# Performance work log

Measured on AMD Instinct MI355X. Metric: run time of the kernel, lower is better.

## Reference

```python
import jax, jax.numpy as jnp
import numpy as np

N = 200000          # total nodes across the batch of graphs
IN_DIM = 320        # pooling_dim (256) + num_context_attrs (64)
POOL_DIM = 256      # output_dim
HID = 128
NUM_GRAPHS = 2000


def setup_inputs() -> dict:
    key = jax.random.key(0)
    k = jax.random.split(key, 6)
    z = jax.random.normal(k[0], (N, IN_DIM), dtype=jnp.float32)
    batch_index = jnp.sort(jax.random.randint(k[1], (N,), 0, NUM_GRAPHS, dtype=jnp.int64))
    # Kaiming-ish small init to keep softmax well-conditioned
    W1 = jax.random.normal(k[2], (HID, IN_DIM), dtype=jnp.float32) * (1.0 / np.sqrt(IN_DIM))
    b1 = jax.random.normal(k[3], (HID,), dtype=jnp.float32) * 0.01
    W2 = jax.random.normal(k[4], (1, HID), dtype=jnp.float32) * (1.0 / np.sqrt(HID))
    b2 = jax.random.normal(k[5], (1,), dtype=jnp.float32) * 0.01
    return {"z": z, "batch_index": batch_index, "W1": W1, "b1": b1,
            "W2": W2, "b2": b2, "num_graphs": NUM_GRAPHS}


def reference(z, batch_index, W1, b1, W2, b2, num_graphs):
    # attention_net: Linear -> ReLU -> Linear, scores: [N, 1]
    h = jax.nn.relu(z @ W1.T + b1)                  # [N, HID]
    scores = h @ W2.T + b2                          # [N, 1]
    # global (over all nodes) max-subtract + softmax along dim 0
    scores = scores - jnp.max(scores, axis=0, keepdims=True)
    weights = jax.nn.softmax(scores, axis=0)        # [N, 1]
    # weighted scatter-mean over graphs keyed by batch_index
    weighted = weights * z[:, :POOL_DIM]            # [N, POOL_DIM]
    sums = jax.ops.segment_sum(weighted, batch_index, num_segments=num_graphs)  # [G, POOL_DIM]
    counts = jax.ops.segment_sum(jnp.ones((z.shape[0],), dtype=z.dtype),
                                 batch_index, num_segments=num_graphs)          # [G]
    pooled = sums / jnp.maximum(counts, 1.0)[:, None]
    return pooled
```

## Files before the change

kernel.cpp:

```cpp
#include <hip/hip_runtime.h>

#define IN_DIM   320
#define POOL_DIM 256
#define HID      128
#define RPB      128
#define NKC      10

typedef __attribute__((ext_vector_type(8))) short bf16x8;
typedef __attribute__((ext_vector_type(4))) float f32x4;

typedef __attribute__((address_space(1))) const unsigned int guint;
typedef __attribute__((address_space(3))) unsigned int luint;

__device__ __forceinline__ void gl_lds16(const void* g, void* l) {
    __builtin_amdgcn_global_load_lds((guint*)g, (luint*)l, 16, 0, 0);
}

__device__ __forceinline__ unsigned fbits(float f) {
    union { float f; unsigned u; } c; c.f = f; return c.u;
}
__device__ __forceinline__ unsigned pack2(unsigned u0, unsigned u1) {
    return __builtin_amdgcn_perm(u1, u0, 0x07060302u);
}

__device__ __forceinline__ void split8(float4 a, float4 b, bf16x8& hi, bf16x8& lo) {
    float f[8] = { a.x, a.y, a.z, a.w, b.x, b.y, b.z, b.w };
    unsigned hu[8], lu[8];
#pragma unroll
    for (int i = 0; i < 8; ++i) {
        unsigned u = fbits(f[i]);
        hu[i] = u;
        float hif = __builtin_bit_cast(float, u & 0xffff0000u);
        lu[i] = fbits(f[i] - hif);
    }
    int4 hp, lp;
    hp.x = pack2(hu[0], hu[1]); hp.y = pack2(hu[2], hu[3]);
    hp.z = pack2(hu[4], hu[5]); hp.w = pack2(hu[6], hu[7]);
    lp.x = pack2(lu[0], lu[1]); lp.y = pack2(lu[2], lu[3]);
    lp.z = pack2(lu[4], lu[5]); lp.w = pack2(lu[6], lu[7]);
    hi = __builtin_bit_cast(bf16x8, hp);
    lo = __builtin_bit_cast(bf16x8, lp);
}

__global__ __launch_bounds__(256) void pack_w1_kernel(
    const float* __restrict__ W1, ushort* __restrict__ Wpk)
{
    const int i = blockIdx.x * 256 + threadIdx.x;
    if (i >= NKC * 8 * 2 * 64) return;
    const int kc   = i >> 10;
    const int r    = i & 1023;
    const int ht   = r >> 7;
    const int r2   = r & 127;
    const int s    = r2 >> 6;
    const int lane = r2 & 63;
    const int h    = ht * 16 + (lane & 15);
    const int k0   = kc * 32 + (lane >> 4) * 8;

    ushort v[8];
#pragma unroll
    for (int j = 0; j < 8; ++j) {
        const float f = W1[(size_t)h * IN_DIM + k0 + j];
        const unsigned u = fbits(f);
        if (s == 0) {
            v[j] = (ushort)(u >> 16);
        } else {
            const float hif = __builtin_bit_cast(float, u & 0xffff0000u);
            v[j] = (ushort)(fbits(f - hif) >> 16);
        }
    }
    ushort* dst = Wpk + (size_t)i * 8;
#pragma unroll
    for (int j = 0; j < 8; ++j) dst[j] = v[j];
}

__global__ __launch_bounds__(256) void attn_scores_mfma(
    const float* __restrict__ z, const ushort* __restrict__ Wpk,
    const float* __restrict__ b1, const float* __restrict__ W2,
    const float* __restrict__ b2,
    float* __restrict__ scores, float* __restrict__ bmax,
    float* __restrict__ bsum, int N)
{
    __shared__ float4 wbuf[2][1024];
    __shared__ float  sblk[RPB];

    const int tid  = threadIdx.x;
    const int wid  = tid >> 6;
    const int lane = tid & 63;
    const int lm   = lane & 15;
    const int lg   = lane >> 4;
    const int r0   = blockIdx.x * RPB;
    const int wr0  = r0 + wid * 32;

    int row0 = wr0 + lm;      if (row0 > N - 1) row0 = N - 1;
    int row1 = wr0 + 16 + lm; if (row1 > N - 1) row1 = N - 1;
    const float* zp0 = z + (size_t)row0 * IN_DIM + lg * 8;
    const float* zp1 = z + (size_t)row1 * IN_DIM + lg * 8;

    #define STAGE_W(kc_, b_)                                                  \
        { const char* src = (const char*)Wpk + (size_t)(kc_) * 16384;         \
          char* dst = (char*)&wbuf[b_][0];                                    \
          _Pragma("unroll")                                                   \
          for (int j = 0; j < 4; ++j) {                                       \
              const int o = (tid + j * 256) * 16;                             \
              gl_lds16(src + o, dst + o);                                     \
          } }

    f32x4 acc[2][8];
#pragma unroll
    for (int rt = 0; rt < 2; ++rt)
#pragma unroll
        for (int ht = 0; ht < 8; ++ht) acc[rt][ht] = (f32x4){0.f, 0.f, 0.f, 0.f};

    float4 zraw[2][4];
    bf16x8 af[2][4];

    STAGE_W(0, 0);

    {
        const float4* p0 = (const float4*)zp0;
        const float4* p1 = (const float4*)zp1;
        zraw[0][0] = p0[0]; zraw[0][1] = p0[1];
        zraw[0][2] = p1[0]; zraw[0][3] = p1[1];
        const float4* q0 = (const float4*)(zp0 + 32);
        const float4* q1 = (const float4*)(zp1 + 32);
        zraw[1][0] = q0[0]; zraw[1][1] = q0[1];
        zraw[1][2] = q1[0]; zraw[1][3] = q1[1];
        split8(zraw[0][0], zraw[0][1], af[0][0], af[0][1]);
        split8(zraw[0][2], zraw[0][3], af[0][2], af[0][3]);
    }
    __syncthreads();

#pragma unroll
    for (int kc = 0; kc < NKC; ++kc) {
        const int cb  = kc & 1;
        const int nb2 = cb ^ 1;

        if (kc + 1 < NKC) STAGE_W(kc + 1, nb2);

        const char* wb_base = (const char*)&wbuf[cb][0] + lane * 16;
#pragma unroll
        for (int ht = 0; ht < 8; ++ht) {
            const bf16x8 bh = *(const bf16x8*)(wb_base + ht * 2048);
            const bf16x8 bl = *(const bf16x8*)(wb_base + ht * 2048 + 1024);
            acc[0][ht] = __builtin_amdgcn_mfma_f32_16x16x32_bf16(af[cb][0], bh, acc[0][ht], 0, 0, 0);
            acc[0][ht] = __builtin_amdgcn_mfma_f32_16x16x32_bf16(af[cb][1], bh, acc[0][ht], 0, 0, 0);
            acc[0][ht] = __builtin_amdgcn_mfma_f32_16x16x32_bf16(af[cb][0], bl, acc[0][ht], 0, 0, 0);
            acc[1][ht] = __builtin_amdgcn_mfma_f32_16x16x32_bf16(af[cb][2], bh, acc[1][ht], 0, 0, 0);
            acc[1][ht] = __builtin_amdgcn_mfma_f32_16x16x32_bf16(af[cb][3], bh, acc[1][ht], 0, 0, 0);
            acc[1][ht] = __builtin_amdgcn_mfma_f32_16x16x32_bf16(af[cb][2], bl, acc[1][ht], 0, 0, 0);
        }

        if (kc + 2 < NKC) {
            const int ko2 = (kc + 2) * 32;
            const float4* p0 = (const float4*)(zp0 + ko2);
            const float4* p1 = (const float4*)(zp1 + ko2);
            zraw[cb][0] = p0[0]; zraw[cb][1] = p0[1];
            zraw[cb][2] = p1[0]; zraw[cb][3] = p1[1];
        }

        if (kc + 1 < NKC) {
            split8(zraw[nb2][0], zraw[nb2][1], af[nb2][0], af[nb2][1]);
            split8(zraw[nb2][2], zraw[nb2][3], af[nb2][2], af[nb2][3]);
            __syncthreads();
        }
    }

    float b1v[8], w2v[8];
#pragma unroll
    for (int ht = 0; ht < 8; ++ht) {
        b1v[ht] = b1[ht * 16 + lm];
        w2v[ht] = W2[ht * 16 + lm];
    }
    const float b2v = b2[0];

#pragma unroll
    for (int rt = 0; rt < 2; ++rt) {
#pragma unroll
        for (int reg = 0; reg < 4; ++reg) {
            float s = 0.f;
#pragma unroll
            for (int ht = 0; ht < 8; ++ht)
                s += fmaxf(acc[rt][ht][reg] + b1v[ht], 0.f) * w2v[ht];
            s += __shfl_xor(s, 1);
            s += __shfl_xor(s, 2);
            s += __shfl_xor(s, 4);
            s += __shfl_xor(s, 8);
            s += b2v;
            if (lm == 0) {
                const int rloc = wid * 32 + rt * 16 + lg * 4 + reg;
                const int grow = r0 + rloc;
                if (grow < N) {
                    scores[grow] = s;
                    sblk[rloc] = s;
                } else {
                    sblk[rloc] = -1e30f;
                }
            }
        }
    }
    __syncthreads();

    if (tid < 64) {
        const float v0 = sblk[tid];
        const float v1 = sblk[tid + 64];
        float m = fmaxf(v0, v1);
#pragma unroll
        for (int d = 1; d < 64; d <<= 1) m = fmaxf(m, __shfl_xor(m, d, 64));
        float e = __expf(v0 - m) + __expf(v1 - m);
#pragma unroll
        for (int d = 1; d < 64; d <<= 1) e += __shfl_xor(e, d, 64);
        if (tid == 0) {
            bmax[blockIdx.x] = m;
            bsum[blockIdx.x] = e;
        }
    }
}

__global__ __launch_bounds__(256) void softmax_reduce_kernel(
    const float* __restrict__ bmax, const float* __restrict__ bsum,
    float* __restrict__ red, int nb)
{
    __shared__ float sm[4];
    __shared__ float ss[4];
    const int tid = threadIdx.x;

    float m = -1e30f;
    for (int i = tid; i < nb; i += 256) m = fmaxf(m, bmax[i]);
#pragma unroll
    for (int d = 1; d < 64; d <<= 1) m = fmaxf(m, __shfl_xor(m, d, 64));
    if ((tid & 63) == 0) sm[tid >> 6] = m;
    __syncthreads();
    const float gmax = fmaxf(fmaxf(sm[0], sm[1]), fmaxf(sm[2], sm[3]));

    float s = 0.f;
    for (int i = tid; i < nb; i += 256) s += bsum[i] * __expf(bmax[i] - gmax);
#pragma unroll
    for (int d = 1; d < 64; d <<= 1) s += __shfl_xor(s, d, 64);
    if ((tid & 63) == 0) ss[tid >> 6] = s;
    __syncthreads();
    if (tid == 0) {
        red[0] = gmax;
        red[1] = ss[0] + ss[1] + ss[2] + ss[3];
    }
}

__device__ __forceinline__ int lower_bound(const int* __restrict__ a, int n, int key)
{
    int lo = 0, hi = n;
    while (lo < hi) {
        int mid = (lo + hi) >> 1;
        if (a[mid] < key) lo = mid + 1; else hi = mid;
    }
    return lo;
}

__global__ __launch_bounds__(256) void pool_kernel(
    const float* __restrict__ z, const int* __restrict__ bidx,
    const float* __restrict__ scores, const float* __restrict__ red,
    float* __restrict__ out, int N)
{
    const int g    = blockIdx.x;
    const int lane = threadIdx.x & 63;
    const int rg   = threadIdx.x >> 6;
    __shared__ int se[2];
    __shared__ f32x4 pred[4][64];

    if (threadIdx.x == 0) {
        se[0] = lower_bound(bidx, N, g);
        se[1] = lower_bound(bidx, N, g + 1);
    }
    __syncthreads();
    const int start = se[0], end = se[1];
    const float gmax    = red[0];
    const float inv_den = 1.0f / red[1];

    const f32x4* zf = (const f32x4*)z;

    f32x4 acc = (f32x4){0.f, 0.f, 0.f, 0.f};
    for (int i = start + rg; i < end; i += 4) {
        const float w = __expf(scores[i] - gmax);
        acc += w * zf[(size_t)i * 80 + lane];
    }
    pred[rg][lane] = acc;
    __syncthreads();

    if (rg == 0) {
        const f32x4 s = (pred[0][lane] + pred[1][lane]) +
                        (pred[2][lane] + pred[3][lane]);
        const int cnt = end - start;
        const float sc = inv_den / fmaxf((float)cnt, 1.0f);
        ((f32x4*)out)[(size_t)g * 64 + lane] = s * sc;
    }
}

extern "C" void kernel_launch(void* const* d_in, const int* in_sizes, int n_in,
                              void* d_out, int out_size, void* d_ws, size_t ws_size,
                              hipStream_t stream)
{
    const float* z    = (const float*)d_in[0];
    const int*   bidx = (const int*)  d_in[1];
    const float* W1   = (const float*)d_in[2];
    const float* b1   = (const float*)d_in[3];
    const float* W2   = (const float*)d_in[4];
    const float* b2   = (const float*)d_in[5];
    float*       out  = (float*)d_out;

    const int N  = in_sizes[0] / IN_DIM;
    const int G  = out_size / POOL_DIM;
    const int nb = (N + RPB - 1) / RPB;

    float*  scores = (float*)d_ws;
    float*  bmax   = scores + 200000;
    float*  bsum   = bmax + 1600;
    float*  red    = bsum + 1600;
    ushort* Wpk    = (ushort*)(red + 16);

    pack_w1_kernel<<<(NKC * 8 * 2 * 64 + 255) / 256, 256, 0, stream>>>(W1, Wpk);
    attn_scores_mfma<<<nb, 256, 0, stream>>>(z, Wpk, b1, W2, b2,
                                             scores, bmax, bsum, N);
    softmax_reduce_kernel<<<1, 256, 0, stream>>>(bmax, bsum, red, nb);
    pool_kernel<<<G, 256, 0, stream>>>(z, bidx, scores, red, out, N);
}
```

Baseline: 110.4 us.

## Fuse weighted segment pooling into score kernel with per-block partials

The score kernel now uses the block's sorted batch indices to find graph segments and accumulates exp-weighted partial sums of the pooled features while z rows are still hot. It writes the per-segment partials plus graph ids. A small combine kernel rescales each partial by its block max relative to the global max and sums them per graph. This avoids a second full pass over z in the pool kernel, at the cost of partial-buffer traffic and a serial segment loop per block.

```diff
diff --git a/kernel.cpp b/kernel.cpp
--- a/kernel.cpp
+++ b/kernel.cpp
@@ -5,6 +5,7 @@
 #define HID      128
 #define RPB      128
 #define NKC      10
+#define NSEG     16
 
 typedef __attribute__((ext_vector_type(8))) short bf16x8;
 typedef __attribute__((ext_vector_type(4))) float f32x4;
@@ -73,15 +74,20 @@
     for (int j = 0; j < 8; ++j) dst[j] = v[j];
 }
 
-__global__ __launch_bounds__(256) void attn_scores_mfma(
+__global__ __launch_bounds__(256) void attn_fused(
     const float* __restrict__ z, const ushort* __restrict__ Wpk,
     const float* __restrict__ b1, const float* __restrict__ W2,
-    const float* __restrict__ b2,
-    float* __restrict__ scores, float* __restrict__ bmax,
-    float* __restrict__ bsum, int N)
+    const float* __restrict__ b2, const int* __restrict__ bidx,
+    float* __restrict__ bmax, float* __restrict__ bsum,
+    float* __restrict__ P, int* __restrict__ meta, int N)
 {
     __shared__ float4 wbuf[2][1024];
     __shared__ float  sblk[RPB];
+    __shared__ int    gbid[RPB];
+    __shared__ int    seg_s0[RPB + 1];
+    __shared__ int    seg_gid[RPB];
+    __shared__ int    scnt[2];
+    __shared__ float  mshare;
 
     const int tid  = threadIdx.x;
     const int wid  = tid >> 6;
@@ -90,6 +96,7 @@
     const int lg   = lane >> 4;
     const int r0   = blockIdx.x * RPB;
     const int wr0  = r0 + wid * 32;
+    const int nvalid = (N - r0 < RPB) ? (N - r0) : RPB;
 
     int row0 = wr0 + lm;      if (row0 > N - 1) row0 = N - 1;
     int row1 = wr0 + 16 + lm; if (row1 > N - 1) row1 = N - 1;
@@ -188,13 +195,7 @@
             s += b2v;
             if (lm == 0) {
                 const int rloc = wid * 32 + rt * 16 + lg * 4 + reg;
-                const int grow = r0 + rloc;
-                if (grow < N) {
-                    scores[grow] = s;
-                    sblk[rloc] = s;
-                } else {
-                    sblk[rloc] = -1e30f;
-                }
+                sblk[rloc] = (rloc < nvalid) ? s : -1e30f;
             }
         }
     }
@@ -212,8 +213,53 @@
         if (tid == 0) {
             bmax[blockIdx.x] = m;
             bsum[blockIdx.x] = e;
-        }
-    }
+            mshare = m;
+        }
+    }
+    if (tid >= 128 && tid < 256) {
+        const int row = tid - 128;
+        gbid[row] = (row < nvalid) ? bidx[r0 + row] : -2;
+    }
+    __syncthreads();
+
+    int flag = 0, idx = 0;
+    if (tid < 128) {
+        const int prev = (tid == 0) ? -999999 : gbid[tid - 1];
+        flag = (gbid[tid] != prev) ? 1 : 0;
+        const unsigned long long mask = __ballot(flag);
+        idx = __popcll(mask & ((1ull << (tid & 63)) - 1ull));
+        if ((tid & 63) == 0) scnt[tid >> 6] = (int)__popcll(mask);
+    }
+    __syncthreads();
+    const int nseg = scnt[0] + scnt[1];
+    if (tid < 128 && flag) {
+        const int pos = idx + ((tid >= 64) ? scnt[0] : 0);
+        seg_s0[pos]  = tid;
+        seg_gid[pos] = gbid[tid];
+    }
+    if (tid == 0) seg_s0[nseg] = RPB;
+    __syncthreads();
+
+    const int rg    = tid >> 6;
+    const float mb  = mshare;
+    const f32x4* zf = (const f32x4*)z;
+    f32x4* P4 = (f32x4*)P;
+
+    for (int s = 0; s < nseg && s < NSEG; ++s) {
+        const int gid = seg_gid[s];
+        if (gid < 0) continue;
+        const int rs = seg_s0[s];
+        const int re = seg_s0[s + 1];
+        f32x4 a = (f32x4){0.f, 0.f, 0.f, 0.f};
+        for (int row = rs + rg; row < re; row += 4) {
+            const float w = __expf(sblk[row] - mb);
+            a += w * zf[(size_t)(r0 + row) * 80 + lane];
+        }
+        P4[(((size_t)blockIdx.x * NSEG + s) * 4 + rg) * 64 + lane] = a;
+    }
+    if (tid < NSEG)
+        meta[blockIdx.x * NSEG + tid] =
+            (tid < nseg && tid < NSEG) ? seg_gid[tid] : -1;
 }
 
 __global__ __launch_bounds__(256) void softmax_reduce_kernel(
@@ -254,43 +300,39 @@
     return lo;
 }
 
-__global__ __launch_bounds__(256) void pool_kernel(
-    const float* __restrict__ z, const int* __restrict__ bidx,
-    const float* __restrict__ scores, const float* __restrict__ red,
-    float* __restrict__ out, int N)
+__global__ __launch_bounds__(64) void combine_kernel(
+    const int* __restrict__ bidx, const float* __restrict__ bmax,
+    const float* __restrict__ red, const float* __restrict__ P,
+    const int* __restrict__ meta, float* __restrict__ out, int N)
 {
     const int g    = blockIdx.x;
-    const int lane = threadIdx.x & 63;
-    const int rg   = threadIdx.x >> 6;
-    __shared__ int se[2];
-    __shared__ f32x4 pred[4][64];
-
-    if (threadIdx.x == 0) {
-        se[0] = lower_bound(bidx, N, g);
-        se[1] = lower_bound(bidx, N, g + 1);
-    }
-    __syncthreads();
-    const int start = se[0], end = se[1];
+    const int lane = threadIdx.x;
+
+    const int start = lower_bound(bidx, N, g);
+    const int end   = lower_bound(bidx, N, g + 1);
     const float gmax    = red[0];
     const float inv_den = 1.0f / red[1];
 
-    const f32x4* zf = (const f32x4*)z;
-
-    f32x4 acc = (f32x4){0.f, 0.f, 0.f, 0.f};
-    for (int i = start + rg; i < end; i += 4) {
-        const float w = __expf(scores[i] - gmax);
-        acc += w * zf[(size_t)i * 80 + lane];
-    }
-    pred[rg][lane] = acc;
-    __syncthreads();
-
-    if (rg == 0) {
-        const f32x4 s = (pred[0][lane] + pred[1][lane]) +
-                        (pred[2][lane] + pred[3][lane]);
-        const int cnt = end - start;
-        const float sc = inv_den / fmaxf((float)cnt, 1.0f);
-        ((f32x4*)out)[(size_t)g * 64 + lane] = s * sc;
-    }
+    f32x4 a = (f32x4){0.f, 0.f, 0.f, 0.f};
+    if (end > start) {
+        const int b0 = start >> 7;
+        const int b1 = (end - 1) >> 7;
+        const f32x4* P4 = (const f32x4*)P;
+        for (int b = b0; b <= b1; ++b) {
+            int s = -1;
+#pragma unroll
+            for (int k = 0; k < NSEG; ++k)
+                if (meta[b * NSEG + k] == g) s = k;
+            if (s < 0) continue;
+            const size_t base = (((size_t)b * NSEG + s) * 4) * 64 + lane;
+            const f32x4 t = (P4[base] + P4[base + 64]) +
+                            (P4[base + 128] + P4[base + 192]);
+            a += __expf(bmax[b] - gmax) * t;
+        }
+    }
+    const int cnt = end - start;
+    const float sc = inv_den / fmaxf((float)cnt, 1.0f);
+    ((f32x4*)out)[(size_t)g * 64 + lane] = a * sc;
 }
 
 extern "C" void kernel_launch(void* const* d_in, const int* in_sizes, int n_in,
@@ -309,15 +351,16 @@
     const int G  = out_size / POOL_DIM;
     const int nb = (N + RPB - 1) / RPB;
 
-    float*  scores = (float*)d_ws;
-    float*  bmax   = scores + 200000;
-    float*  bsum   = bmax + 1600;
-    float*  red    = bsum + 1600;
-    ushort* Wpk    = (ushort*)(red + 16);
+    float*  bmax = (float*)d_ws;
+    float*  bsum = bmax + 1600;
+    float*  red  = bsum + 1600;
+    int*    meta = (int*)(red + 16);
+    float*  P    = (float*)(meta + 1600 * NSEG);
+    ushort* Wpk  = (ushort*)(P + (size_t)1600 * NSEG * 4 * 256);
 
     pack_w1_kernel<<<(NKC * 8 * 2 * 64 + 255) / 256, 256, 0, stream>>>(W1, Wpk);
-    attn_scores_mfma<<<nb, 256, 0, stream>>>(z, Wpk, b1, W2, b2,
-                                             scores, bmax, bsum, N);
+    attn_fused<<<nb, 256, 0, stream>>>(z, Wpk, b1, W2, b2, bidx,
+                                       bmax, bsum, P, meta, N);
     softmax_reduce_kernel<<<1, 256, 0, stream>>>(bmax, bsum, red, nb);
-    pool_kernel<<<G, 256, 0, stream>>>(z, bidx, scores, red, out, N);
-}
+    combine_kernel<<<G, 64, 0, stream>>>(bidx, bmax, red, P, meta, out, N);
+}
```

Result: slower. 122.5 us (+11.0%).

## Stage z tiles into LDS via async global_load_lds with XOR swizzle

Applied to the files above, without the earlier changes.

Moves the z activation loads from per-lane register prefetch into double-buffered LDS staging with direct global-to-LDS loads, using coalesced row-contiguous copies and an XOR swizzle to avoid bank conflicts on readback. Each k-chunk then reads its fragments from LDS and splits them to bf16 hi/lo before the MFMAs. This is meant to improve global coalescing and cut register pressure from the raw prefetch buffers. In exchange it adds 32KB of LDS per block, which may lower occupancy, and puts the split on the critical path after each barrier.

```diff
diff --git a/kernel.cpp b/kernel.cpp
--- a/kernel.cpp
+++ b/kernel.cpp
@@ -81,6 +81,7 @@
     float* __restrict__ bsum, int N)
 {
     __shared__ float4 wbuf[2][1024];
+    __shared__ float4 zbuf[2][1024];
     __shared__ float  sblk[RPB];
 
     const int tid  = threadIdx.x;
@@ -89,12 +90,16 @@
     const int lm   = lane & 15;
     const int lg   = lane >> 4;
     const int r0   = blockIdx.x * RPB;
-    const int wr0  = r0 + wid * 32;
-
-    int row0 = wr0 + lm;      if (row0 > N - 1) row0 = N - 1;
-    int row1 = wr0 + 16 + lm; if (row1 > N - 1) row1 = N - 1;
-    const float* zp0 = z + (size_t)row0 * IN_DIM + lg * 8;
-    const float* zp1 = z + (size_t)row1 * IN_DIM + lg * 8;
+
+    const char* zsrc[4];
+#pragma unroll
+    for (int j = 0; j < 4; ++j) {
+        const int s   = tid + j * 256;
+        const int row = s >> 3;
+        const int q   = (s & 7) ^ (row & 7);
+        int gr = r0 + row; if (gr > N - 1) gr = N - 1;
+        zsrc[j] = (const char*)z + (size_t)gr * (IN_DIM * 4) + q * 16;
+    }
 
     #define STAGE_W(kc_, b_)                                                  \
         { const char* src = (const char*)Wpk + (size_t)(kc_) * 16384;         \
@@ -105,29 +110,29 @@
               gl_lds16(src + o, dst + o);                                     \
           } }
 
+    #define STAGE_Z(kc_, b_)                                                  \
+        { char* dst = (char*)&zbuf[b_][0];                                    \
+          _Pragma("unroll")                                                   \
+          for (int j = 0; j < 4; ++j) {                                       \
+              const int o = (tid + j * 256) * 16;                             \
+              gl_lds16(zsrc[j] + (kc_) * 128, dst + o);                       \
+          } }
+
     f32x4 acc[2][8];
 #pragma unroll
     for (int rt = 0; rt < 2; ++rt)
 #pragma unroll
         for (int ht = 0; ht < 8; ++ht) acc[rt][ht] = (f32x4){0.f, 0.f, 0.f, 0.f};
 
-    float4 zraw[2][4];
-    bf16x8 af[2][4];
-
+    const int lr0 = wid * 32 + lm;
+    const int lr1 = lr0 + 16;
+    const int i00 = lr0 * 8 + ((2 * lg)     ^ (lr0 & 7));
+    const int i01 = lr0 * 8 + ((2 * lg + 1) ^ (lr0 & 7));
+    const int i10 = lr1 * 8 + ((2 * lg)     ^ (lr1 & 7));
+    const int i11 = lr1 * 8 + ((2 * lg + 1) ^ (lr1 & 7));
+
+    STAGE_Z(0, 0);
     STAGE_W(0, 0);
-
-    {
-        const float4* p0 = (const float4*)zp0;
-        const float4* p1 = (const float4*)zp1;
-        zraw[0][0] = p0[0]; zraw[0][1] = p0[1];
-        zraw[0][2] = p1[0]; zraw[0][3] = p1[1];
-        const float4* q0 = (const float4*)(zp0 + 32);
-        const float4* q1 = (const float4*)(zp1 + 32);
-        zraw[1][0] = q0[0]; zraw[1][1] = q0[1];
-        zraw[1][2] = q1[0]; zraw[1][3] = q1[1];
-        split8(zraw[0][0], zraw[0][1], af[0][0], af[0][1]);
-        split8(zraw[0][2], zraw[0][3], af[0][2], af[0][3]);
-    }
     __syncthreads();
 
 #pragma unroll
@@ -135,34 +140,36 @@
         const int cb  = kc & 1;
         const int nb2 = cb ^ 1;
 
-        if (kc + 1 < NKC) STAGE_W(kc + 1, nb2);
+        if (kc + 1 < NKC) {
+            STAGE_Z(kc + 1, nb2);
+            STAGE_W(kc + 1, nb2);
+        }
+
+        bf16x8 a0h, a0l, a1h, a1l;
+        {
+            const float4* zb = &zbuf[cb][0];
+            const float4 x0 = zb[i00];
+            const float4 x1 = zb[i01];
+            const float4 y0 = zb[i10];
+            const float4 y1 = zb[i11];
+            split8(x0, x1, a0h, a0l);
+            split8(y0, y1, a1h, a1l);
+        }
 
         const char* wb_base = (const char*)&wbuf[cb][0] + lane * 16;
 #pragma unroll
         for (int ht = 0; ht < 8; ++ht) {
             const bf16x8 bh = *(const bf16x8*)(wb_base + ht * 2048);
             const bf16x8 bl = *(const bf16x8*)(wb_base + ht * 2048 + 1024);
-            acc[0][ht] = __builtin_amdgcn_mfma_f32_16x16x32_bf16(af[cb][0], bh, acc[0][ht], 0, 0, 0);
-            acc[0][ht] = __builtin_amdgcn_mfma_f32_16x16x32_bf16(af[cb][1], bh, acc[0][ht], 0, 0, 0);
-            acc[0][ht] = __builtin_amdgcn_mfma_f32_16x16x32_bf16(af[cb][0], bl, acc[0][ht], 0, 0, 0);
-            acc[1][ht] = __builtin_amdgcn_mfma_f32_16x16x32_bf16(af[cb][2], bh, acc[1][ht], 0, 0, 0);
-            acc[1][ht] = __builtin_amdgcn_mfma_f32_16x16x32_bf16(af[cb][3], bh, acc[1][ht], 0, 0, 0);
-            acc[1][ht] = __builtin_amdgcn_mfma_f32_16x16x32_bf16(af[cb][2], bl, acc[1][ht], 0, 0, 0);
-        }
-
-        if (kc + 2 < NKC) {
-            const int ko2 = (kc + 2) * 32;
-            const float4* p0 = (const float4*)(zp0 + ko2);
-            const float4* p1 = (const float4*)(zp1 + ko2);
-            zraw[cb][0] = p0[0]; zraw[cb][1] = p0[1];
-            zraw[cb][2] = p1[0]; zraw[cb][3] = p1[1];
-        }
-
-        if (kc + 1 < NKC) {
-            split8(zraw[nb2][0], zraw[nb2][1], af[nb2][0], af[nb2][1]);
-            split8(zraw[nb2][2], zraw[nb2][3], af[nb2][2], af[nb2][3]);
-            __syncthreads();
-        }
+            acc[0][ht] = __builtin_amdgcn_mfma_f32_16x16x32_bf16(a0h, bh, acc[0][ht], 0, 0, 0);
+            acc[0][ht] = __builtin_amdgcn_mfma_f32_16x16x32_bf16(a0l, bh, acc[0][ht], 0, 0, 0);
+            acc[0][ht] = __builtin_amdgcn_mfma_f32_16x16x32_bf16(a0h, bl, acc[0][ht], 0, 0, 0);
+            acc[1][ht] = __builtin_amdgcn_mfma_f32_16x16x32_bf16(a1h, bh, acc[1][ht], 0, 0, 0);
+            acc[1][ht] = __builtin_amdgcn_mfma_f32_16x16x32_bf16(a1l, bh, acc[1][ht], 0, 0, 0);
+            acc[1][ht] = __builtin_amdgcn_mfma_f32_16x16x32_bf16(a1h, bl, acc[1][ht], 0, 0, 0);
+        }
+
+        if (kc + 1 < NKC) __syncthreads();
     }
 
     float b1v[8], w2v[8];
```

Result: slower. 116.8 us (+5.8%).

## Deepen z prefetch to three stages and fold softmax reduce into pool kernel

Applied to the files above, without the earlier changes.

The attention-score kernel now keeps three register buffers of raw z and loads chunk kc+3 while computing chunk kc, which hides more global-load latency at the cost of extra VGPRs. The separate single-block softmax reduction kernel is removed. Every pool block now recomputes the global max and denominator from the 1563 per-block partials, trading one launch and its serial gap for redundant small reductions in all 2000 blocks.

```diff
diff --git a/kernel.cpp b/kernel.cpp
--- a/kernel.cpp
+++ b/kernel.cpp
@@ -111,20 +111,19 @@
 #pragma unroll
         for (int ht = 0; ht < 8; ++ht) acc[rt][ht] = (f32x4){0.f, 0.f, 0.f, 0.f};
 
-    float4 zraw[2][4];
+    float4 zraw[3][4];
     bf16x8 af[2][4];
 
     STAGE_W(0, 0);
 
     {
-        const float4* p0 = (const float4*)zp0;
-        const float4* p1 = (const float4*)zp1;
-        zraw[0][0] = p0[0]; zraw[0][1] = p0[1];
-        zraw[0][2] = p1[0]; zraw[0][3] = p1[1];
-        const float4* q0 = (const float4*)(zp0 + 32);
-        const float4* q1 = (const float4*)(zp1 + 32);
-        zraw[1][0] = q0[0]; zraw[1][1] = q0[1];
-        zraw[1][2] = q1[0]; zraw[1][3] = q1[1];
+#pragma unroll
+        for (int c = 0; c < 3; ++c) {
+            const float4* p0 = (const float4*)(zp0 + c * 32);
+            const float4* p1 = (const float4*)(zp1 + c * 32);
+            zraw[c][0] = p0[0]; zraw[c][1] = p0[1];
+            zraw[c][2] = p1[0]; zraw[c][3] = p1[1];
+        }
         split8(zraw[0][0], zraw[0][1], af[0][0], af[0][1]);
         split8(zraw[0][2], zraw[0][3], af[0][2], af[0][3]);
     }
@@ -150,17 +149,18 @@
             acc[1][ht] = __builtin_amdgcn_mfma_f32_16x16x32_bf16(af[cb][2], bl, acc[1][ht], 0, 0, 0);
         }
 
-        if (kc + 2 < NKC) {
-            const int ko2 = (kc + 2) * 32;
-            const float4* p0 = (const float4*)(zp0 + ko2);
-            const float4* p1 = (const float4*)(zp1 + ko2);
-            zraw[cb][0] = p0[0]; zraw[cb][1] = p0[1];
-            zraw[cb][2] = p1[0]; zraw[cb][3] = p1[1];
+        if (kc + 3 < NKC) {
+            const int ko3 = (kc + 3) * 32;
+            const float4* p0 = (const float4*)(zp0 + ko3);
+            const float4* p1 = (const float4*)(zp1 + ko3);
+            zraw[kc % 3][0] = p0[0]; zraw[kc % 3][1] = p0[1];
+            zraw[kc % 3][2] = p1[0]; zraw[kc % 3][3] = p1[1];
         }
 
         if (kc + 1 < NKC) {
-            split8(zraw[nb2][0], zraw[nb2][1], af[nb2][0], af[nb2][1]);
-            split8(zraw[nb2][2], zraw[nb2][3], af[nb2][2], af[nb2][3]);
+            const int zn = (kc + 1) % 3;
+            split8(zraw[zn][0], zraw[zn][1], af[nb2][0], af[nb2][1]);
+            split8(zraw[zn][2], zraw[zn][3], af[nb2][2], af[nb2][3]);
             __syncthreads();
         }
     }
@@ -216,34 +216,6 @@
     }
 }
 
-__global__ __launch_bounds__(256) void softmax_reduce_kernel(
-    const float* __restrict__ bmax, const float* __restrict__ bsum,
-    float* __restrict__ red, int nb)
-{
-    __shared__ float sm[4];
-    __shared__ float ss[4];
-    const int tid = threadIdx.x;
-
-    float m = -1e30f;
-    for (int i = tid; i < nb; i += 256) m = fmaxf(m, bmax[i]);
-#pragma unroll
-    for (int d = 1; d < 64; d <<= 1) m = fmaxf(m, __shfl_xor(m, d, 64));
-    if ((tid & 63) == 0) sm[tid >> 6] = m;
-    __syncthreads();
-    const float gmax = fmaxf(fmaxf(sm[0], sm[1]), fmaxf(sm[2], sm[3]));
-
-    float s = 0.f;
-    for (int i = tid; i < nb; i += 256) s += bsum[i] * __expf(bmax[i] - gmax);
-#pragma unroll
-    for (int d = 1; d < 64; d <<= 1) s += __shfl_xor(s, d, 64);
-    if ((tid & 63) == 0) ss[tid >> 6] = s;
-    __syncthreads();
-    if (tid == 0) {
-        red[0] = gmax;
-        red[1] = ss[0] + ss[1] + ss[2] + ss[3];
-    }
-}
-
 __device__ __forceinline__ int lower_bound(const int* __restrict__ a, int n, int key)
 {
     int lo = 0, hi = n;
@@ -256,24 +228,40 @@
 
 __global__ __launch_bounds__(256) void pool_kernel(
     const float* __restrict__ z, const int* __restrict__ bidx,
-    const float* __restrict__ scores, const float* __restrict__ red,
-    float* __restrict__ out, int N)
+    const float* __restrict__ scores, const float* __restrict__ bmax,
+    const float* __restrict__ bsum, float* __restrict__ out, int N, int nbk)
 {
     const int g    = blockIdx.x;
-    const int lane = threadIdx.x & 63;
-    const int rg   = threadIdx.x >> 6;
-    __shared__ int se[2];
+    const int tid  = threadIdx.x;
+    const int lane = tid & 63;
+    const int rg   = tid >> 6;
+    __shared__ int   se[2];
+    __shared__ float sm[4];
+    __shared__ float ss[4];
     __shared__ f32x4 pred[4][64];
 
-    if (threadIdx.x == 0) {
+    float m = -1e30f;
+    for (int i = tid; i < nbk; i += 256) m = fmaxf(m, bmax[i]);
+#pragma unroll
+    for (int d = 1; d < 64; d <<= 1) m = fmaxf(m, __shfl_xor(m, d, 64));
+    if (lane == 0) sm[rg] = m;
+    if (tid == 0) {
         se[0] = lower_bound(bidx, N, g);
         se[1] = lower_bound(bidx, N, g + 1);
     }
     __syncthreads();
+    const float gmax = fmaxf(fmaxf(sm[0], sm[1]), fmaxf(sm[2], sm[3]));
+
+    float sden = 0.f;
+    for (int i = tid; i < nbk; i += 256) sden += bsum[i] * __expf(bmax[i] - gmax);
+#pragma unroll
+    for (int d = 1; d < 64; d <<= 1) sden += __shfl_xor(sden, d, 64);
+    if (lane == 0) ss[rg] = sden;
+    __syncthreads();
+    const float den = (ss[0] + ss[1]) + (ss[2] + ss[3]);
+    const float inv_den = 1.0f / den;
+
     const int start = se[0], end = se[1];
-    const float gmax    = red[0];
-    const float inv_den = 1.0f / red[1];
-
     const f32x4* zf = (const f32x4*)z;
 
     f32x4 acc = (f32x4){0.f, 0.f, 0.f, 0.f};
@@ -312,12 +300,10 @@
     float*  scores = (float*)d_ws;
     float*  bmax   = scores + 200000;
     float*  bsum   = bmax + 1600;
-    float*  red    = bsum + 1600;
-    ushort* Wpk    = (ushort*)(red + 16);
+    ushort* Wpk    = (ushort*)(bsum + 1600);
 
     pack_w1_kernel<<<(NKC * 8 * 2 * 64 + 255) / 256, 256, 0, stream>>>(W1, Wpk);
     attn_scores_mfma<<<nb, 256, 0, stream>>>(z, Wpk, b1, W2, b2,
                                              scores, bmax, bsum, N);
-    softmax_reduce_kernel<<<1, 256, 0, stream>>>(bmax, bsum, red, nb);
-    pool_kernel<<<G, 256, 0, stream>>>(z, bidx, scores, red, out, N);
-}
+    pool_kernel<<<G, 256, 0, stream>>>(z, bidx, scores, bmax, bsum, out, N, nb);
+}
```

After: 123.8 us. 1.12x slower.
